# Kernel optimization log

Measured on AMD Instinct MI355X. Metric: run time of the kernel, lower is better.

## Reference

```python
import jax, jax.numpy as jnp
import numpy as np

NUM_CLASSES = 80
NUM_TOP_QUERIES = 300


def setup_inputs() -> dict:
    key = jax.random.key(0)
    k1, k2, k3 = jax.random.split(key, 3)
    B, Q, C, K = 512, 900, NUM_CLASSES, 17
    return {
        "pred_logits": jax.random.normal(k1, (B, Q, C), dtype=jnp.float32),
        "pred_boxes": jax.random.uniform(k2, (B, Q, 4), dtype=jnp.float32),
        "pred_keypoints": jax.random.uniform(k3, (B, Q, K, 2), dtype=jnp.float32),
    }


def reference(pred_logits, pred_boxes, pred_keypoints):
    # focal-loss branch of DFINEPostProcessor.forward
    B = pred_logits.shape[0]
    C = NUM_CLASSES
    scores = jax.nn.sigmoid(pred_logits)            # [B, Q, C]
    flat = scores.reshape(B, -1)                    # [B, Q*C]
    top_scores, idx = jax.lax.top_k(flat, NUM_TOP_QUERIES)  # [B, T]
    labels = idx % C                                # mod(index, num_classes)
    qidx = idx // C                                 # query index
    # gather selected boxes / keypoints per batch element
    boxes = jnp.take_along_axis(pred_boxes, qidx[:, :, None], axis=1)            # [B, T, 4]
    kpts = jnp.take_along_axis(pred_keypoints, qidx[:, :, None, None], axis=1)   # [B, T, K, 2]
    return labels, boxes, top_scores, kpts
```

## Files before the change

kernel.cpp:

```cpp
#include <hip/hip_runtime.h>
#include <stdint.h>

#define NB 512
#define NQ 900
#define NC 80
#define NK 17
#define QC 72000
#define TOPT 300
#define NTHREADS 1024
#define MAXCAND 2560
#define NBINS 2048
#define BIN_BASE 0x40000000u
#define BIN_SHIFT 13
#define MAXSEL 512

__global__ __launch_bounds__(NTHREADS, 8) void dfine_topk(
    const float* __restrict__ logits,
    const float* __restrict__ boxes,
    const float* __restrict__ kpts,
    float* __restrict__ out_labels,
    float* __restrict__ out_boxes,
    float* __restrict__ out_scores,
    float* __restrict__ out_kpts)
{
    __shared__ uint32_t hist[NBINS];
    __shared__ uint32_t cand_bits[MAXCAND];
    __shared__ uint32_t cand_idx[MAXCAND];
    __shared__ unsigned long long sel[MAXSEL];
    __shared__ uint32_t wsums[16];
    __shared__ uint32_t s_qidx[TOPT];
    __shared__ uint32_t s_cnt, s_sel_cnt, s_thr;

    const int tid = threadIdx.x;
    const int b   = blockIdx.x;

    for (int i = tid; i < NBINS; i += NTHREADS) hist[i] = 0;
    if (tid == 0) { s_cnt = 0; s_sel_cnt = 0; s_thr = BIN_BASE; }
    __syncthreads();

    const float4* lg4 = (const float4*)(logits + (size_t)b * QC);

    auto process = [&](float4 v, int i) {
        int b0 = __float_as_int(v.x);
        int b1 = __float_as_int(v.y);
        int b2 = __float_as_int(v.z);
        int b3 = __float_as_int(v.w);
        if (b0 >= (int)BIN_BASE || b1 >= (int)BIN_BASE ||
            b2 >= (int)BIN_BASE || b3 >= (int)BIN_BASE) {
            int bitsArr[4] = {b0, b1, b2, b3};
            #pragma unroll
            for (int j = 0; j < 4; ++j) {
                int bits = bitsArr[j];
                if (bits >= (int)BIN_BASE) {
                    uint32_t p = atomicAdd(&s_cnt, 1u);
                    if (p < MAXCAND) {
                        cand_bits[p] = (uint32_t)bits;
                        cand_idx[p]  = (uint32_t)(i * 4 + j);
                        uint32_t bin = ((uint32_t)bits - BIN_BASE) >> BIN_SHIFT;
                        if (bin >= NBINS) bin = NBINS - 1;
                        atomicAdd(&hist[bin], 1u);
                    }
                }
            }
        }
    };

    const int N4 = QC / 4;
    int base = 0;
    for (; base + 2 * NTHREADS <= N4; base += 2 * NTHREADS) {
        float4 v0 = lg4[base + tid];
        float4 v1 = lg4[base + tid + NTHREADS];
        process(v0, base + tid);
        process(v1, base + tid + NTHREADS);
    }
    for (int i = base + tid; i < N4; i += NTHREADS) {
        float4 v = lg4[i];
        process(v, i);
    }
    __syncthreads();

    uint32_t cnt = s_cnt; if (cnt > MAXCAND) cnt = MAXCAND;

    {
        uint32_t ps = hist[2 * tid] + hist[2 * tid + 1];
        uint32_t x = ps;
        const int lane = tid & 63;
        #pragma unroll
        for (int d = 1; d < 64; d <<= 1) {
            uint32_t y = __shfl_down(x, d, 64);
            if (lane + d < 64) x += y;
        }
        int wid = tid >> 6;
        if (lane == 0) wsums[wid] = x;
        __syncthreads();
        uint32_t off = 0;
        for (int w = wid + 1; w < 16; ++w) off += wsums[w];
        uint32_t incl = x + off;
        uint32_t excl = incl - ps;
        if (excl < TOPT && incl >= TOPT) {
            int bsel;
            uint32_t c = excl + hist[2 * tid + 1];
            if (c >= TOPT) bsel = 2 * tid + 1;
            else           bsel = 2 * tid;
            int thrbin = bsel - 1;
            if (thrbin < 0) thrbin = 0;
            s_thr = BIN_BASE + ((uint32_t)thrbin << BIN_SHIFT);
        }
        __syncthreads();
    }

    uint32_t thr = s_thr;
    for (int i = tid; i < (int)cnt; i += NTHREADS) {
        uint32_t bitsu = cand_bits[i];
        if (bitsu >= thr) {
            float x = __uint_as_float(bitsu);
            float u = expf(-x);
            float s = 1.0f / (1.0f + u);
            uint32_t sb = __float_as_uint(s);
            uint32_t p = atomicAdd(&s_sel_cnt, 1u);
            if (p < MAXSEL)
                sel[p] = ((unsigned long long)sb << 32) | (uint32_t)(~cand_idx[i]);
        }
    }
    __syncthreads();

    uint32_t nsel = s_sel_cnt; if (nsel > MAXSEL) nsel = MAXSEL;

    unsigned long long K = 0ull;
    if (tid < 512 && tid < (int)nsel) K = sel[tid];
    __syncthreads();

    for (int k = 2; k <= 512; k <<= 1) {
        for (int j = k >> 1; j > 0; j >>= 1) {
            bool asc   = ((tid & k) == 0);
            bool lower = ((tid & j) == 0);
            unsigned long long other = 0ull;
            if (j >= 64) {
                if (tid < 512) sel[tid] = K;
                __syncthreads();
                if (tid < 512) other = sel[tid ^ j];
                __syncthreads();
            } else {
                other = __shfl_xor(K, j, 64);
            }
            if (tid < 512) {
                bool sw = lower ? ((K < other) == asc)
                                : ((other < K) == asc);
                if (sw) K = other;
            }
        }
    }
    if (tid < 512) sel[tid] = K;
    __syncthreads();

    float* oL = out_labels + (size_t)b * TOPT;
    float* oS = out_scores + (size_t)b * TOPT;
    for (int r = tid; r < TOPT; r += NTHREADS) {
        unsigned long long key = sel[r];
        uint32_t sb  = (uint32_t)(key >> 32);
        uint32_t idx = ~((uint32_t)key);
        if (key == 0ull) { sb = 0; idx = 0; }
        uint32_t q   = idx / NC;
        uint32_t lab = idx - q * NC;
        oL[r] = (float)lab;
        oS[r] = __uint_as_float(sb);
        s_qidx[r] = q;
    }
    __syncthreads();

    const float4* ib4 = (const float4*)(boxes + (size_t)b * NQ * 4);
    float4* ob4 = (float4*)(out_boxes + (size_t)b * TOPT * 4);
    for (int r = tid; r < TOPT; r += NTHREADS) ob4[r] = ib4[s_qidx[r]];

    const float2* ik2 = (const float2*)(kpts + (size_t)b * NQ * NK * 2);
    float2* ok2 = (float2*)(out_kpts + (size_t)b * TOPT * NK * 2);
    for (int i = tid; i < TOPT * NK; i += NTHREADS) {
        int r = i / NK;
        int j = i - r * NK;
        ok2[(size_t)r * NK + j] = ik2[(size_t)s_qidx[r] * NK + j];
    }
}

extern "C" void kernel_launch(void* const* d_in, const int* in_sizes, int n_in,
                              void* d_out, int out_size, void* d_ws, size_t ws_size,
                              hipStream_t stream) {
    const float* logits = (const float*)d_in[0];
    const float* boxes  = (const float*)d_in[1];
    const float* kpts   = (const float*)d_in[2];
    float* out = (float*)d_out;
    float* oL = out;
    float* oB = oL + (size_t)NB * TOPT;
    float* oS = oB + (size_t)NB * TOPT * 4;
    float* oK = oS + (size_t)NB * TOPT;
    dfine_topk<<<NB, NTHREADS, 0, stream>>>(logits, boxes, kpts, oL, oB, oS, oK);
}
```

Measured before the change: 259.9 us.

## Use wave-aggregated candidate compaction and defer histogram build to a second pass

The candidate filter now builds a per-thread bitmask over four float4 loads and compacts indices with a wave prefix sum and one shared atomic per wave, replacing per-element shared atomics. Candidate values are then re-read from global memory by index in a separate pass that also builds the histogram. The main loop is unrolled to four loads per thread. This cuts atomic contention in the streaming pass, at the cost of an extra gather from global/L2 and an added barrier.

Result: no change. 261.6 us (+0.7%).

```diff
diff --git a/kernel.cpp b/kernel.cpp
--- a/kernel.cpp
+++ b/kernel.cpp
@@ -24,67 +24,90 @@
     float* __restrict__ out_kpts)
 {
     __shared__ uint32_t hist[NBINS];
+    __shared__ uint32_t cand_idx[MAXCAND];
     __shared__ uint32_t cand_bits[MAXCAND];
-    __shared__ uint32_t cand_idx[MAXCAND];
     __shared__ unsigned long long sel[MAXSEL];
     __shared__ uint32_t wsums[16];
     __shared__ uint32_t s_qidx[TOPT];
     __shared__ uint32_t s_cnt, s_sel_cnt, s_thr;
 
-    const int tid = threadIdx.x;
-    const int b   = blockIdx.x;
+    const int tid  = threadIdx.x;
+    const int b    = blockIdx.x;
+    const int lane = tid & 63;
 
     for (int i = tid; i < NBINS; i += NTHREADS) hist[i] = 0;
     if (tid == 0) { s_cnt = 0; s_sel_cnt = 0; s_thr = BIN_BASE; }
     __syncthreads();
 
     const float4* lg4 = (const float4*)(logits + (size_t)b * QC);
-
-    auto process = [&](float4 v, int i) {
-        int b0 = __float_as_int(v.x);
-        int b1 = __float_as_int(v.y);
-        int b2 = __float_as_int(v.z);
-        int b3 = __float_as_int(v.w);
-        if (b0 >= (int)BIN_BASE || b1 >= (int)BIN_BASE ||
-            b2 >= (int)BIN_BASE || b3 >= (int)BIN_BASE) {
-            int bitsArr[4] = {b0, b1, b2, b3};
-            #pragma unroll
-            for (int j = 0; j < 4; ++j) {
-                int bits = bitsArr[j];
-                if (bits >= (int)BIN_BASE) {
-                    uint32_t p = atomicAdd(&s_cnt, 1u);
-                    if (p < MAXCAND) {
-                        cand_bits[p] = (uint32_t)bits;
-                        cand_idx[p]  = (uint32_t)(i * 4 + j);
-                        uint32_t bin = ((uint32_t)bits - BIN_BASE) >> BIN_SHIFT;
-                        if (bin >= NBINS) bin = NBINS - 1;
-                        atomicAdd(&hist[bin], 1u);
-                    }
-                }
-            }
-        }
+    const int N4 = QC / 4;
+
+    auto mask4 = [&](float4 v) -> uint32_t {
+        uint32_t r = 0;
+        r |= (uint32_t)(__float_as_int(v.x) >= (int)BIN_BASE);
+        r |= (uint32_t)(__float_as_int(v.y) >= (int)BIN_BASE) << 1;
+        r |= (uint32_t)(__float_as_int(v.z) >= (int)BIN_BASE) << 2;
+        r |= (uint32_t)(__float_as_int(v.w) >= (int)BIN_BASE) << 3;
+        return r;
     };
 
-    const int N4 = QC / 4;
+    auto flush = [&](uint32_t m, uint32_t i0) {
+        uint32_t c = (uint32_t)__popc(m);
+        uint32_t x = c;
+        #pragma unroll
+        for (int d = 1; d < 64; d <<= 1) {
+            uint32_t y = __shfl_up(x, d, 64);
+            if (lane >= d) x += y;
+        }
+        uint32_t tot = __shfl(x, 63, 64);
+        uint32_t wb = 0;
+        if (lane == 0 && tot) wb = atomicAdd(&s_cnt, tot);
+        wb = __shfl(wb, 0, 64);
+        uint32_t pos = wb + x - c;
+        while (m) {
+            int k = __ffs(m) - 1;
+            m &= m - 1;
+            if (pos < MAXCAND)
+                cand_idx[pos] = i0 + ((uint32_t)(k >> 2) << 12) + (uint32_t)(k & 3);
+            ++pos;
+        }
+    };
+
     int base = 0;
-    for (; base + 2 * NTHREADS <= N4; base += 2 * NTHREADS) {
+    for (; base + 4 * NTHREADS <= N4; base += 4 * NTHREADS) {
         float4 v0 = lg4[base + tid];
         float4 v1 = lg4[base + tid + NTHREADS];
-        process(v0, base + tid);
-        process(v1, base + tid + NTHREADS);
-    }
-    for (int i = base + tid; i < N4; i += NTHREADS) {
-        float4 v = lg4[i];
-        process(v, i);
+        float4 v2 = lg4[base + tid + 2 * NTHREADS];
+        float4 v3 = lg4[base + tid + 3 * NTHREADS];
+        uint32_t m = mask4(v0) | (mask4(v1) << 4) | (mask4(v2) << 8) | (mask4(v3) << 12);
+        flush(m, (uint32_t)(base + tid) * 4u);
+    }
+    for (int i0u = base; i0u < N4; i0u += NTHREADS) {
+        int i = i0u + tid;
+        uint32_t m = 0;
+        if (i < N4) m = mask4(lg4[i]);
+        flush(m, (uint32_t)i * 4u);
     }
     __syncthreads();
 
     uint32_t cnt = s_cnt; if (cnt > MAXCAND) cnt = MAXCAND;
+
+    {
+        const float* lg = logits + (size_t)b * QC;
+        for (int i = tid; i < (int)cnt; i += NTHREADS) {
+            uint32_t idx  = cand_idx[i];
+            uint32_t bits = __float_as_uint(lg[idx]);
+            cand_bits[i] = bits;
+            uint32_t bin = (bits - BIN_BASE) >> BIN_SHIFT;
+            if (bin >= NBINS) bin = NBINS - 1;
+            atomicAdd(&hist[bin], 1u);
+        }
+        __syncthreads();
+    }
 
     {
         uint32_t ps = hist[2 * tid] + hist[2 * tid + 1];
         uint32_t x = ps;
-        const int lane = tid & 63;
         #pragma unroll
         for (int d = 1; d < 64; d <<= 1) {
             uint32_t y = __shfl_down(x, d, 64);
```
